# Kernel tuning notes

Hardware: AMD Instinct MI355X
Metric: run time of the kernel (lower is better)

## Reference

```python
import jax, jax.numpy as jnp
import numpy as np

N, IN_DIM, OUT_DIM = 8192, 256, 64
NEG_BIG = -9e15
LRELU_SLOPE = 0.01  # torch F.leaky_relu default


def setup_inputs() -> dict:
    key = jax.random.key(0)
    k1, k2, k3, k4 = jax.random.split(key, 4)
    inp = jax.random.normal(k1, (N, IN_DIM), dtype=jnp.float32)
    adj = jax.random.randint(k2, (N, N), 0, 2, dtype=jnp.int32)
    # xavier_uniform with gain=1.414
    limW = 1.414 * np.sqrt(6.0 / (IN_DIM + OUT_DIM))
    W = jax.random.uniform(k3, (IN_DIM, OUT_DIM), minval=-limW, maxval=limW, dtype=jnp.float32)
    lima = 1.414 * np.sqrt(6.0 / (2 * OUT_DIM + 1))
    a = jax.random.uniform(k4, (2 * OUT_DIM, 1), minval=-lima, maxval=lima, dtype=jnp.float32)
    return {"input": inp, "adj": adj, "W": W, "a": a}


def reference(input, adj, W, a):
    h = input @ W                      # [N, D]
    a1, a2 = a[:OUT_DIM, 0], a[OUT_DIM:, 0]
    # e[i,j] = leaky_relu(a1.h_i + a2.h_j) == the concat-based score, no NxNx2D tensor
    f1 = h @ a1                        # [N]
    f2 = h @ a2                        # [N]
    e = jax.nn.leaky_relu(f1[:, None] + f2[None, :], negative_slope=LRELU_SLOPE)  # [N, N]
    face_Rhand = e[1, 2]
    face_Lhand = e[1, 3]
    Rhand_Lhand = e[3, 2]
    attention = jnp.where(adj > 0, e, jnp.float32(NEG_BIG))
    alpha = jax.nn.softmax(attention, axis=1)
    h_prime = alpha @ h                # [N, D]
    return (h_prime, face_Rhand, face_Lhand, Rhand_Lhand)
```

## Files before the change

kernel.cpp:

```cpp
#include <hip/hip_runtime.h>
#include <hip/hip_bf16.h>

#define GN 8192
#define KD 256
#define OD 64
#define LOG2E 1.44269504f

typedef __attribute__((ext_vector_type(8))) short bf16x8;
typedef __attribute__((ext_vector_type(4))) float f32x4;

__device__ __forceinline__ float fexp2(float x) {
#if __has_builtin(__builtin_amdgcn_exp2f)
  return __builtin_amdgcn_exp2f(x);
#else
  return exp2f(x);
#endif
}

__global__ __launch_bounds__(256) void gat_k1(
    const float* __restrict__ input, const float* __restrict__ W,
    const float* __restrict__ a, __hip_bfloat16* __restrict__ hT,
    float* __restrict__ f1p, float* __restrict__ f2p, float* __restrict__ out)
{
  __shared__ float Wl[KD * OD];
  __shared__ float inT[KD * 33];
  __shared__ float red1[8][32];
  __shared__ float red2[8][32];
  __shared__ float s1row[32];
  __shared__ float s2row[32];

  const int tid = threadIdx.x;
  const int i0 = blockIdx.x * 32;

  for (int idx = tid; idx < KD * OD / 4; idx += 256)
    ((float4*)Wl)[idx] = ((const float4*)W)[idx];

#pragma unroll
  for (int it = 0; it < 8; ++it) {
    int idx = tid + it * 256;
    int r = idx >> 6, k4 = idx & 63;
    float4 v = *(const float4*)(input + (long)(i0 + r) * KD + k4 * 4);
    inT[(k4 * 4 + 0) * 33 + r] = v.x;
    inT[(k4 * 4 + 1) * 33 + r] = v.y;
    inT[(k4 * 4 + 2) * 33 + r] = v.z;
    inT[(k4 * 4 + 3) * 33 + r] = v.w;
  }
  __syncthreads();

  const int r = tid & 31;
  const int cg = tid >> 5;
  float acc[8];
#pragma unroll
  for (int c = 0; c < 8; ++c) acc[c] = 0.f;

#pragma unroll 4
  for (int k = 0; k < KD; ++k) {
    float inv = inT[k * 33 + r];
    float4 wa = *(const float4*)&Wl[k * 64 + cg * 8];
    float4 wb = *(const float4*)&Wl[k * 64 + cg * 8 + 4];
    acc[0] += inv * wa.x; acc[1] += inv * wa.y;
    acc[2] += inv * wa.z; acc[3] += inv * wa.w;
    acc[4] += inv * wb.x; acc[5] += inv * wb.y;
    acc[6] += inv * wb.z; acc[7] += inv * wb.w;
  }

#pragma unroll
  for (int c = 0; c < 8; ++c)
    hT[(long)(cg * 8 + c) * GN + i0 + r] = __float2bfloat16(acc[c]);

  float s1 = 0.f, s2 = 0.f;
#pragma unroll
  for (int c = 0; c < 8; ++c) {
    s1 += acc[c] * a[cg * 8 + c];
    s2 += acc[c] * a[OD + cg * 8 + c];
  }
  red1[cg][r] = s1; red2[cg][r] = s2;
  __syncthreads();
  if (tid < 32) {
    float f1 = 0.f, f2 = 0.f;
#pragma unroll
    for (int g = 0; g < 8; ++g) { f1 += red1[g][tid]; f2 += red2[g][tid]; }
    s1row[tid] = f1; s2row[tid] = f2;
    f1p[i0 + tid] = f1 * LOG2E;
    f2p[i0 + tid] = f2 * LOG2E;
  }
  __syncthreads();
  if (blockIdx.x == 0 && tid == 0) {
    float e12 = s1row[1] + s2row[2];
    float e13 = s1row[1] + s2row[3];
    float e32 = s1row[3] + s2row[2];
    out[(long)GN * OD + 0] = fmaxf(e12, 0.01f * e12);
    out[(long)GN * OD + 1] = fmaxf(e13, 0.01f * e13);
    out[(long)GN * OD + 2] = fmaxf(e32, 0.01f * e32);
  }
}

__global__ __launch_bounds__(512, 4) void gat_k2(
    const int* __restrict__ adj, const __hip_bfloat16* __restrict__ hT,
    const float* __restrict__ f1p, const float* __restrict__ f2p,
    float* __restrict__ out)
{
  __shared__ float pbuf[8][16][66];
  __shared__ float sbuf[8][16];

  const int tid = threadIdx.x;
  const int lane = tid & 63;
  const int wv = tid >> 6;
  const int tn = lane & 15;
  const int quad = lane >> 4;
  const int i0 = blockIdx.x * 16;
  const int jbase = wv * 1024;

  const float f1r = f1p[i0 + tn];

  f32x4 acc[4];
#pragma unroll
  for (int nf = 0; nf < 4; ++nf) acc[nf] = (f32x4){0.f, 0.f, 0.f, 0.f};
  f32x4 accS = (f32x4){0.f, 0.f, 0.f, 0.f};

  bf16x8 ones;
  {
    short ov = (tn == 0) ? (short)0x3F80 : (short)0;
#pragma unroll
    for (int i = 0; i < 8; ++i) ones[i] = ov;
  }

  const int* ap = adj + (long)(i0 + tn) * GN + jbase + quad * 8;
  const float* fp = f2p + jbase + quad * 8;
  const __hip_bfloat16* hp = hT + (long)tn * GN + jbase + quad * 8;

  int4 A0[2], A1[2];
  float4 F0[2], F1[2];
  bf16x8 B[2][4];

  A0[0] = *(const int4*)ap;
  A1[0] = *(const int4*)(ap + 4);
  F0[0] = *(const float4*)fp;
  F1[0] = *(const float4*)(fp + 4);
#pragma unroll
  for (int g = 0; g < 4; ++g)
    B[0][g] = *(const bf16x8*)(hp + (long)g * (16 * GN));

#pragma unroll
  for (int c = 0; c < 32; ++c) {
    const int cur = c & 1, nxt = cur ^ 1;
    if (c + 1 < 32) {
      A0[nxt] = *(const int4*)(ap + (c + 1) * 32);
      A1[nxt] = *(const int4*)(ap + (c + 1) * 32 + 4);
      F0[nxt] = *(const float4*)(fp + (c + 1) * 32);
      F1[nxt] = *(const float4*)(fp + (c + 1) * 32 + 4);
#pragma unroll
      for (int g = 0; g < 4; ++g)
        B[nxt][g] = *(const bf16x8*)(hp + (long)g * (16 * GN) + (c + 1) * 32);
    }

    const int4 ca0 = A0[cur], ca1 = A1[cur];
    const float4 cF0 = F0[cur], cF1 = F1[cur];
    float e0 = f1r + cF0.x, e1 = f1r + cF0.y, e2 = f1r + cF0.z, e3 = f1r + cF0.w;
    float e4 = f1r + cF1.x, e5 = f1r + cF1.y, e6 = f1r + cF1.z, e7 = f1r + cF1.w;
    float m0 = fmaxf(e0, 0.01f * e0), m1 = fmaxf(e1, 0.01f * e1);
    float m2 = fmaxf(e2, 0.01f * e2), m3 = fmaxf(e3, 0.01f * e3);
    float m4 = fmaxf(e4, 0.01f * e4), m5 = fmaxf(e5, 0.01f * e5);
    float m6 = fmaxf(e6, 0.01f * e6), m7 = fmaxf(e7, 0.01f * e7);
    float w0 = fexp2((ca0.x > 0) ? m0 : -256.f);
    float w1 = fexp2((ca0.y > 0) ? m1 : -256.f);
    float w2 = fexp2((ca0.z > 0) ? m2 : -256.f);
    float w3 = fexp2((ca0.w > 0) ? m3 : -256.f);
    float w4 = fexp2((ca1.x > 0) ? m4 : -256.f);
    float w5 = fexp2((ca1.y > 0) ? m5 : -256.f);
    float w6 = fexp2((ca1.z > 0) ? m6 : -256.f);
    float w7 = fexp2((ca1.w > 0) ? m7 : -256.f);

    union { bf16x8 v; unsigned u[4]; } wf;
    wf.u[0] = __builtin_amdgcn_perm(__float_as_uint(w1), __float_as_uint(w0), 0x07060302u);
    wf.u[1] = __builtin_amdgcn_perm(__float_as_uint(w3), __float_as_uint(w2), 0x07060302u);
    wf.u[2] = __builtin_amdgcn_perm(__float_as_uint(w5), __float_as_uint(w4), 0x07060302u);
    wf.u[3] = __builtin_amdgcn_perm(__float_as_uint(w7), __float_as_uint(w6), 0x07060302u);

    acc[0] = __builtin_amdgcn_mfma_f32_16x16x32_bf16(wf.v, B[cur][0], acc[0], 0, 0, 0);
    acc[1] = __builtin_amdgcn_mfma_f32_16x16x32_bf16(wf.v, B[cur][1], acc[1], 0, 0, 0);
    acc[2] = __builtin_amdgcn_mfma_f32_16x16x32_bf16(wf.v, B[cur][2], acc[2], 0, 0, 0);
    acc[3] = __builtin_amdgcn_mfma_f32_16x16x32_bf16(wf.v, B[cur][3], acc[3], 0, 0, 0);
    accS   = __builtin_amdgcn_mfma_f32_16x16x32_bf16(wf.v, ones,      accS,   0, 0, 0);
  }

#pragma unroll
  for (int nf = 0; nf < 4; ++nf)
#pragma unroll
    for (int rg = 0; rg < 4; ++rg)
      pbuf[wv][quad * 4 + rg][nf * 16 + tn] = acc[nf][rg];
  if (tn == 0) {
#pragma unroll
    for (int rg = 0; rg < 4; ++rg)
      sbuf[wv][quad * 4 + rg] = accS[rg];
  }
  __syncthreads();
  for (int t = tid; t < 16 * OD; t += 512) {
    int rr = t >> 6, cc = t & 63;
    float num = 0.f, den = 0.f;
#pragma unroll
    for (int w = 0; w < 8; ++w) { num += pbuf[w][rr][cc]; den += sbuf[w][rr]; }
    out[(long)(i0 + rr) * OD + cc] = num / den;
  }
}

extern "C" void kernel_launch(void* const* d_in, const int* in_sizes, int n_in,
                              void* d_out, int out_size, void* d_ws, size_t ws_size,
                              hipStream_t stream) {
  const float* input = (const float*)d_in[0];
  const int* adj     = (const int*)d_in[1];
  const float* W     = (const float*)d_in[2];
  const float* a     = (const float*)d_in[3];
  float* out = (float*)d_out;

  __hip_bfloat16* hT = (__hip_bfloat16*)d_ws;
  float* f1p = (float*)((char*)d_ws + (size_t)OD * GN * sizeof(__hip_bfloat16));
  float* f2p = f1p + GN;

  gat_k1<<<256, 256, 0, stream>>>(input, W, a, hT, f1p, f2p, out);
  gat_k2<<<512, 512, 0, stream>>>(adj, hT, f1p, f2p, out);
}
```

Baseline: 433.1 us.

## Stage adjacency tiles through LDS with coalesced loads and double buffering

The attention kernel now loads 16x256 adjacency tiles with fully coalesced row-contiguous global reads and stages them in double-buffered LDS. Each of four waves then reads its slices from LDS, and all waves sweep the same column range in step, sharing f2 and hT reads. Before, each wave read its own strided 1024-column range straight from global memory. Block size drops to 256 threads and a barrier is added per chunk, which trades some occupancy and register-prefetch overlap of the hT and f2 loads for better coalescing of the dominant adjacency stream.

```diff
diff --git a/kernel.cpp b/kernel.cpp
--- a/kernel.cpp
+++ b/kernel.cpp
@@ -5,6 +5,7 @@
 #define KD 256
 #define OD 64
 #define LOG2E 1.44269504f
+#define ASTR 264
 
 typedef __attribute__((ext_vector_type(8))) short bf16x8;
 typedef __attribute__((ext_vector_type(4))) float f32x4;
@@ -95,13 +96,14 @@
   }
 }
 
-__global__ __launch_bounds__(512, 4) void gat_k2(
+__global__ __launch_bounds__(256, 2) void gat_k2(
     const int* __restrict__ adj, const __hip_bfloat16* __restrict__ hT,
     const float* __restrict__ f1p, const float* __restrict__ f2p,
     float* __restrict__ out)
 {
-  __shared__ float pbuf[8][16][66];
-  __shared__ float sbuf[8][16];
+  __shared__ int abuf[2][16 * ASTR];
+  __shared__ float pb[4][16][68];
+  __shared__ float sb[4][16];
 
   const int tid = threadIdx.x;
   const int lane = tid & 63;
@@ -109,9 +111,16 @@
   const int tn = lane & 15;
   const int quad = lane >> 4;
   const int i0 = blockIdx.x * 16;
-  const int jbase = wv * 1024;
+
+  const int sr = tid >> 4;
+  const int sc = (tid & 15) * 4;
+  const int* gsrc = adj + (long)(i0 + sr) * GN + sc;
 
   const float f1r = f1p[i0 + tn];
+
+  const int jo0 = (2 * wv) * 32 + quad * 8;
+  const int jo1 = (2 * wv + 1) * 32 + quad * 8;
+  const __hip_bfloat16* hbase = hT + (long)tn * GN;
 
   f32x4 acc[4];
 #pragma unroll
@@ -125,81 +134,102 @@
     for (int i = 0; i < 8; ++i) ones[i] = ov;
   }
 
-  const int* ap = adj + (long)(i0 + tn) * GN + jbase + quad * 8;
-  const float* fp = f2p + jbase + quad * 8;
-  const __hip_bfloat16* hp = hT + (long)tn * GN + jbase + quad * 8;
-
-  int4 A0[2], A1[2];
-  float4 F0[2], F1[2];
-  bf16x8 B[2][4];
-
-  A0[0] = *(const int4*)ap;
-  A1[0] = *(const int4*)(ap + 4);
-  F0[0] = *(const float4*)fp;
-  F1[0] = *(const float4*)(fp + 4);
-#pragma unroll
-  for (int g = 0; g < 4; ++g)
-    B[0][g] = *(const bf16x8*)(hp + (long)g * (16 * GN));
-
-#pragma unroll
+  int4 st[4];
+#pragma unroll
+  for (int k = 0; k < 4; ++k) st[k] = *(const int4*)(gsrc + 64 * k);
+#pragma unroll
+  for (int k = 0; k < 4; ++k) *(int4*)&abuf[0][sr * ASTR + sc + 64 * k] = st[k];
+  __syncthreads();
+
   for (int c = 0; c < 32; ++c) {
     const int cur = c & 1, nxt = cur ^ 1;
-    if (c + 1 < 32) {
-      A0[nxt] = *(const int4*)(ap + (c + 1) * 32);
-      A1[nxt] = *(const int4*)(ap + (c + 1) * 32 + 4);
-      F0[nxt] = *(const float4*)(fp + (c + 1) * 32);
-      F1[nxt] = *(const float4*)(fp + (c + 1) * 32 + 4);
-#pragma unroll
-      for (int g = 0; g < 4; ++g)
-        B[nxt][g] = *(const bf16x8*)(hp + (long)g * (16 * GN) + (c + 1) * 32);
-    }
-
-    const int4 ca0 = A0[cur], ca1 = A1[cur];
-    const float4 cF0 = F0[cur], cF1 = F1[cur];
-    float e0 = f1r + cF0.x, e1 = f1r + cF0.y, e2 = f1r + cF0.z, e3 = f1r + cF0.w;
-    float e4 = f1r + cF1.x, e5 = f1r + cF1.y, e6 = f1r + cF1.z, e7 = f1r + cF1.w;
-    float m0 = fmaxf(e0, 0.01f * e0), m1 = fmaxf(e1, 0.01f * e1);
-    float m2 = fmaxf(e2, 0.01f * e2), m3 = fmaxf(e3, 0.01f * e3);
-    float m4 = fmaxf(e4, 0.01f * e4), m5 = fmaxf(e5, 0.01f * e5);
-    float m6 = fmaxf(e6, 0.01f * e6), m7 = fmaxf(e7, 0.01f * e7);
-    float w0 = fexp2((ca0.x > 0) ? m0 : -256.f);
-    float w1 = fexp2((ca0.y > 0) ? m1 : -256.f);
-    float w2 = fexp2((ca0.z > 0) ? m2 : -256.f);
-    float w3 = fexp2((ca0.w > 0) ? m3 : -256.f);
-    float w4 = fexp2((ca1.x > 0) ? m4 : -256.f);
-    float w5 = fexp2((ca1.y > 0) ? m5 : -256.f);
-    float w6 = fexp2((ca1.z > 0) ? m6 : -256.f);
-    float w7 = fexp2((ca1.w > 0) ? m7 : -256.f);
-
-    union { bf16x8 v; unsigned u[4]; } wf;
-    wf.u[0] = __builtin_amdgcn_perm(__float_as_uint(w1), __float_as_uint(w0), 0x07060302u);
-    wf.u[1] = __builtin_amdgcn_perm(__float_as_uint(w3), __float_as_uint(w2), 0x07060302u);
-    wf.u[2] = __builtin_amdgcn_perm(__float_as_uint(w5), __float_as_uint(w4), 0x07060302u);
-    wf.u[3] = __builtin_amdgcn_perm(__float_as_uint(w7), __float_as_uint(w6), 0x07060302u);
-
-    acc[0] = __builtin_amdgcn_mfma_f32_16x16x32_bf16(wf.v, B[cur][0], acc[0], 0, 0, 0);
-    acc[1] = __builtin_amdgcn_mfma_f32_16x16x32_bf16(wf.v, B[cur][1], acc[1], 0, 0, 0);
-    acc[2] = __builtin_amdgcn_mfma_f32_16x16x32_bf16(wf.v, B[cur][2], acc[2], 0, 0, 0);
-    acc[3] = __builtin_amdgcn_mfma_f32_16x16x32_bf16(wf.v, B[cur][3], acc[3], 0, 0, 0);
-    accS   = __builtin_amdgcn_mfma_f32_16x16x32_bf16(wf.v, ones,      accS,   0, 0, 0);
+    if (c < 31) {
+#pragma unroll
+      for (int k = 0; k < 4; ++k)
+        st[k] = *(const int4*)(gsrc + (c + 1) * 256 + 64 * k);
+    }
+
+    const int4 a0 = *(const int4*)&abuf[cur][tn * ASTR + jo0];
+    const int4 a1 = *(const int4*)&abuf[cur][tn * ASTR + jo0 + 4];
+    const int4 a2 = *(const int4*)&abuf[cur][tn * ASTR + jo1];
+    const int4 a3 = *(const int4*)&abuf[cur][tn * ASTR + jo1 + 4];
+    const float4 f20 = *(const float4*)(f2p + c * 256 + jo0);
+    const float4 f21 = *(const float4*)(f2p + c * 256 + jo0 + 4);
+    const float4 f22 = *(const float4*)(f2p + c * 256 + jo1);
+    const float4 f23 = *(const float4*)(f2p + c * 256 + jo1 + 4);
+    bf16x8 B0[4], B1[4];
+#pragma unroll
+    for (int nf = 0; nf < 4; ++nf) {
+      B0[nf] = *(const bf16x8*)(hbase + (long)nf * (16 * GN) + c * 256 + jo0);
+      B1[nf] = *(const bf16x8*)(hbase + (long)nf * (16 * GN) + c * 256 + jo1);
+    }
+
+    union { bf16x8 v; unsigned u[4]; } w0, w1;
+    {
+      float e0 = f1r + f20.x, e1 = f1r + f20.y, e2 = f1r + f20.z, e3 = f1r + f20.w;
+      float e4 = f1r + f21.x, e5 = f1r + f21.y, e6 = f1r + f21.z, e7 = f1r + f21.w;
+      float v0 = fexp2((a0.x > 0) ? fmaxf(e0, 0.01f * e0) : -256.f);
+      float v1 = fexp2((a0.y > 0) ? fmaxf(e1, 0.01f * e1) : -256.f);
+      float v2 = fexp2((a0.z > 0) ? fmaxf(e2, 0.01f * e2) : -256.f);
+      float v3 = fexp2((a0.w > 0) ? fmaxf(e3, 0.01f * e3) : -256.f);
+      float v4 = fexp2((a1.x > 0) ? fmaxf(e4, 0.01f * e4) : -256.f);
+      float v5 = fexp2((a1.y > 0) ? fmaxf(e5, 0.01f * e5) : -256.f);
+      float v6 = fexp2((a1.z > 0) ? fmaxf(e6, 0.01f * e6) : -256.f);
+      float v7 = fexp2((a1.w > 0) ? fmaxf(e7, 0.01f * e7) : -256.f);
+      w0.u[0] = __builtin_amdgcn_perm(__float_as_uint(v1), __float_as_uint(v0), 0x07060302u);
+      w0.u[1] = __builtin_amdgcn_perm(__float_as_uint(v3), __float_as_uint(v2), 0x07060302u);
+      w0.u[2] = __builtin_amdgcn_perm(__float_as_uint(v5), __float_as_uint(v4), 0x07060302u);
+      w0.u[3] = __builtin_amdgcn_perm(__float_as_uint(v7), __float_as_uint(v6), 0x07060302u);
+    }
+    {
+      float e0 = f1r + f22.x, e1 = f1r + f22.y, e2 = f1r + f22.z, e3 = f1r + f22.w;
+      float e4 = f1r + f23.x, e5 = f1r + f23.y, e6 = f1r + f23.z, e7 = f1r + f23.w;
+      float v0 = fexp2((a2.x > 0) ? fmaxf(e0, 0.01f * e0) : -256.f);
+      float v1 = fexp2((a2.y > 0) ? fmaxf(e1, 0.01f * e1) : -256.f);
+      float v2 = fexp2((a2.z > 0) ? fmaxf(e2, 0.01f * e2) : -256.f);
+      float v3 = fexp2((a2.w > 0) ? fmaxf(e3, 0.01f * e3) : -256.f);
+      float v4 = fexp2((a3.x > 0) ? fmaxf(e4, 0.01f * e4) : -256.f);
+      float v5 = fexp2((a3.y > 0) ? fmaxf(e5, 0.01f * e5) : -256.f);
+      float v6 = fexp2((a3.z > 0) ? fmaxf(e6, 0.01f * e6) : -256.f);
+      float v7 = fexp2((a3.w > 0) ? fmaxf(e7, 0.01f * e7) : -256.f);
+      w1.u[0] = __builtin_amdgcn_perm(__float_as_uint(v1), __float_as_uint(v0), 0x07060302u);
+      w1.u[1] = __builtin_amdgcn_perm(__float_as_uint(v3), __float_as_uint(v2), 0x07060302u);
+      w1.u[2] = __builtin_amdgcn_perm(__float_as_uint(v5), __float_as_uint(v4), 0x07060302u);
+      w1.u[3] = __builtin_amdgcn_perm(__float_as_uint(v7), __float_as_uint(v6), 0x07060302u);
+    }
+
+#pragma unroll
+    for (int nf = 0; nf < 4; ++nf)
+      acc[nf] = __builtin_amdgcn_mfma_f32_16x16x32_bf16(w0.v, B0[nf], acc[nf], 0, 0, 0);
+    accS = __builtin_amdgcn_mfma_f32_16x16x32_bf16(w0.v, ones, accS, 0, 0, 0);
+#pragma unroll
+    for (int nf = 0; nf < 4; ++nf)
+      acc[nf] = __builtin_amdgcn_mfma_f32_16x16x32_bf16(w1.v, B1[nf], acc[nf], 0, 0, 0);
+    accS = __builtin_amdgcn_mfma_f32_16x16x32_bf16(w1.v, ones, accS, 0, 0, 0);
+
+    if (c < 31) {
+#pragma unroll
+      for (int k = 0; k < 4; ++k)
+        *(int4*)&abuf[nxt][sr * ASTR + sc + 64 * k] = st[k];
+    }
+    __syncthreads();
   }
 
 #pragma unroll
   for (int nf = 0; nf < 4; ++nf)
 #pragma unroll
     for (int rg = 0; rg < 4; ++rg)
-      pbuf[wv][quad * 4 + rg][nf * 16 + tn] = acc[nf][rg];
+      pb[wv][quad * 4 + rg][nf * 16 + tn] = acc[nf][rg];
   if (tn == 0) {
 #pragma unroll
     for (int rg = 0; rg < 4; ++rg)
-      sbuf[wv][quad * 4 + rg] = accS[rg];
-  }
-  __syncthreads();
-  for (int t = tid; t < 16 * OD; t += 512) {
+      sb[wv][quad * 4 + rg] = accS[rg];
+  }
+  __syncthreads();
+  for (int t = tid; t < 16 * OD; t += 256) {
     int rr = t >> 6, cc = t & 63;
-    float num = 0.f, den = 0.f;
-#pragma unroll
-    for (int w = 0; w < 8; ++w) { num += pbuf[w][rr][cc]; den += sbuf[w][rr]; }
+    float num = pb[0][rr][cc] + pb[1][rr][cc] + pb[2][rr][cc] + pb[3][rr][cc];
+    float den = sb[0][rr] + sb[1][rr] + sb[2][rr] + sb[3][rr];
     out[(long)(i0 + rr) * OD + cc] = num / den;
   }
 }
@@ -218,5 +248,5 @@
   float* f2p = f1p + GN;
 
   gat_k1<<<256, 256, 0, stream>>>(input, W, a, hT, f1p, f2p, out);
-  gat_k2<<<512, 512, 0, stream>>>(adj, hT, f1p, f2p, out);
-}
+  gat_k2<<<512, 256, 0, stream>>>(adj, hT, f1p, f2p, out);
+}
```

After: 392.6 us. -9.4%, faster.
